# Kernel tuning notes

Measured on AMD Instinct MI355X. Metric: run time of the kernel, lower is better.

## Reference

```python
import jax, jax.numpy as jnp
import numpy as np

WINDOW = (8, 8)
NUM_HEADS = 12


def setup_inputs() -> dict:
    key = jax.random.key(0)
    k0, k1, k2 = jax.random.split(key, 3)
    B_, H, W, C = 8, 64, 64, 768
    x = jax.random.normal(k0, (B_, H * W, C), dtype=jnp.float32)
    qkv_w = jax.random.normal(k1, (3 * C, C), dtype=jnp.float32) * 0.02
    qkv_b = jnp.zeros((3 * C,), dtype=jnp.float32)
    proj_w = jax.random.normal(k2, (C, C), dtype=jnp.float32) * 0.02
    proj_b = jnp.zeros((C,), dtype=jnp.float32)
    return {"x": x, "qkv_w": qkv_w, "qkv_b": qkv_b,
            "proj_w": proj_w, "proj_b": proj_b, "H": H, "W": W}


def reference(x, qkv_w, qkv_b, proj_w, proj_b, H, W):
    ws0, ws1 = WINDOW
    nh = NUM_HEADS
    B_, N, C = x.shape
    hd = C // nh
    scale = hd ** (-0.5)

    x = x.reshape(B_, H, W, C)
    # pad bottom/right so H, W divisible by window size (static Python ints)
    pad_b = (ws0 - H % ws0) % ws0
    pad_r = (ws1 - W % ws1) % ws1
    x = jnp.pad(x, ((0, 0), (0, pad_b), (0, pad_r), (0, 0)))
    Hp, Wp = H + pad_b, W + pad_r

    # window partition: (B, Hp, Wp, C) -> (B*nW, ws0*ws1, C)
    xw = (x.reshape(B_, Hp // ws0, ws0, Wp // ws1, ws1, C)
            .transpose(0, 1, 3, 2, 4, 5)
            .reshape(-1, ws0 * ws1, C))
    Bw, Nw = xw.shape[0], xw.shape[1]

    # fused qkv projection
    qkv = xw @ qkv_w.T + qkv_b                       # (Bw, Nw, 3C)
    qkv = qkv.reshape(Bw, Nw, 3, nh, hd).transpose(2, 0, 3, 1, 4)
    q, k, v = qkv[0], qkv[1], qkv[2]                 # (Bw, nh, Nw, hd)

    attn = jax.nn.softmax((q * scale) @ jnp.swapaxes(k, -2, -1), axis=-1)
    out = (attn @ v).transpose(0, 2, 1, 3).reshape(Bw, Nw, C)
    out = out @ proj_w.T + proj_b

    # window reverse: (B*nW, ws0*ws1, C) -> (B, Hp, Wp, C)
    out = (out.reshape(B_, Hp // ws0, Wp // ws1, ws0, ws1, C)
              .transpose(0, 1, 3, 2, 4, 5)
              .reshape(B_, Hp, Wp, C))
    out = out[:, :H, :W, :]
    return out.reshape(B_, H * W, C)
```

## Files before the change

kernel.cpp:

```cpp
#include <hip/hip_runtime.h>
#include <stdint.h>

typedef __attribute__((ext_vector_type(8))) __bf16 bf16x8;
typedef __attribute__((ext_vector_type(4))) float f32x4;
typedef __attribute__((ext_vector_type(8))) unsigned short u16x8;
typedef __attribute__((ext_vector_type(2))) unsigned int u32x2;

__device__ __forceinline__ unsigned short f2bf(float f) {
  union { float f; unsigned u; } v; v.f = f;
  return (unsigned short)((v.u + 0x7FFFu + ((v.u >> 16) & 1u)) >> 16);
}

__device__ __forceinline__ void gload16(const void* g, void* l) {
  __builtin_amdgcn_global_load_lds(
      (const __attribute__((address_space(1))) void*)g,
      (__attribute__((address_space(3))) void*)l, 16, 0, 0);
}

__global__ __launch_bounds__(256) void pack_x_kernel(const float* __restrict__ x,
                                                     unsigned short* __restrict__ xw) {
  int idx = blockIdx.x * 256 + threadIdx.x;
  int m = idx / 96;
  int p = idx - m * 96;
  int win = m >> 6, tok = m & 63;
  int b = win >> 6, wh = (win >> 3) & 7, ww = win & 7;
  int r = tok >> 3, c = tok & 7;
  size_t xoff = ((size_t)b * 4096 + (wh * 8 + r) * 64 + (ww * 8 + c)) * 768 + p * 8;
  const float* src = x + xoff;
  u16x8 o;
#pragma unroll
  for (int j = 0; j < 8; ++j) o[j] = f2bf(src[j]);
  *(u16x8*)(xw + (size_t)m * 768 + p * 8) = o;
}

__global__ __launch_bounds__(256) void pack_w_kernel(const float* __restrict__ qkvw,
                                                     const float* __restrict__ projw,
                                                     unsigned short* __restrict__ wq,
                                                     unsigned short* __restrict__ wp) {
  int idx = blockIdx.x * 256 + threadIdx.x;
  const float* src;
  unsigned short* dst;
  if (idx < 221184) { src = qkvw + (size_t)idx * 8; dst = wq + (size_t)idx * 8; }
  else { int i2 = idx - 221184; src = projw + (size_t)i2 * 8; dst = wp + (size_t)i2 * 8; }
  u16x8 o;
#pragma unroll
  for (int j = 0; j < 8; ++j) o[j] = f2bf(src[j]);
  *(u16x8*)dst = o;
}

template <int N, bool PROJ>
__global__ __launch_bounds__(512, 2) void gemm256_kernel(
    const unsigned short* __restrict__ A, const unsigned short* __restrict__ Bm,
    const float* __restrict__ bias, void* __restrict__ Cout) {
  constexpr int K = 768;
  constexpr int NT = K / 32;
  constexpr int NBN = N / 256;
  extern __shared__ char smem[];

  const int tid = threadIdx.x;
  const int wave = tid >> 6;
  const int lane = tid & 63;
  const int wm = wave >> 2;
  const int wn = wave & 3;

  const int cpx = gridDim.x >> 3;
  const int bid = (blockIdx.x & 7) * cpx + (blockIdx.x >> 3);
  const int tm = (bid / NBN) * 256;
  const int tn = (bid % NBN) * 256;

  const int c0 = tid, c1 = 512 + tid;
  const int r0 = c0 >> 2, r1 = c1 >> 2;
  const int g0 = ((c0 & 3) ^ ((c0 >> 3) & 3)) * 8;
  const int g1 = ((c1 & 3) ^ ((c1 >> 3) & 3)) * 8;
  const unsigned short* gA0 = A + (size_t)(tm + r0) * K + g0;
  const unsigned short* gA1 = A + (size_t)(tm + r1) * K + g1;
  const unsigned short* gB0 = Bm + (size_t)(tn + r0) * K + g0;
  const unsigned short* gB1 = Bm + (size_t)(tn + r1) * K + g1;
  const int ldsA0 = wave * 1024;
  const int ldsA1 = 8192 + wave * 1024;
  const int ldsB0 = 16384 + wave * 1024;
  const int ldsB1 = 24576 + wave * 1024;

  const int lrow = lane & 15;
  const int lg8 = ((lane >> 4) ^ ((lane >> 1) & 3)) * 8;

  {
    char* s0 = smem;
    char* s1 = smem + 32768;
    gload16(gA0, s0 + ldsA0); gload16(gA1, s0 + ldsA1);
    gload16(gB0, s0 + ldsB0); gload16(gB1, s0 + ldsB1);
    gload16(gA0 + 32, s1 + ldsA0); gload16(gA1 + 32, s1 + ldsA1);
    gload16(gB0 + 32, s1 + ldsB0); gload16(gB1 + 32, s1 + ldsB1);
  }
  asm volatile("s_waitcnt vmcnt(4)" ::: "memory");
  asm volatile("s_barrier" ::: "memory");

  f32x4 acc[8][4] = {};

  bf16x8 a0[4], b[4];
  {
    const unsigned short* s0 = (const unsigned short*)smem;
#pragma unroll
    for (int mi = 0; mi < 4; ++mi)
      a0[mi] = *(const bf16x8*)(s0 + (wm * 128 + mi * 16 + lrow) * 32 + lg8);
#pragma unroll
    for (int ni = 0; ni < 4; ++ni)
      b[ni] = *(const bf16x8*)(s0 + 8192 + (wn * 64 + ni * 16 + lrow) * 32 + lg8);
  }

#pragma unroll
  for (int t = 0; t < NT; ++t) {
    const unsigned short* sAt = (const unsigned short*)(smem + ((t & 3) << 15));

    if (t + 2 < NT) {
      char* sb = smem + (((t + 2) & 3) << 15);
      gload16(gA0 + (t + 2) * 32, sb + ldsA0);
      gload16(gA1 + (t + 2) * 32, sb + ldsA1);
    }
    bf16x8 a1[4];
#pragma unroll
    for (int mi = 0; mi < 4; ++mi)
      a1[mi] = *(const bf16x8*)(sAt + (wm * 128 + 64 + mi * 16 + lrow) * 32 + lg8);

    __builtin_amdgcn_s_setprio(1);
#pragma unroll
    for (int mi = 0; mi < 4; ++mi)
#pragma unroll
      for (int ni = 0; ni < 4; ++ni)
        acc[mi][ni] = __builtin_amdgcn_mfma_f32_16x16x32_bf16(b[ni], a0[mi], acc[mi][ni], 0, 0, 0);
    __builtin_amdgcn_s_setprio(0);

    if (t + 2 < NT) {
      char* sb = smem + (((t + 2) & 3) << 15);
      gload16(gB0 + (t + 2) * 32, sb + ldsB0);
      gload16(gB1 + (t + 2) * 32, sb + ldsB1);
    }
    if (t < NT - 2)
      asm volatile("s_waitcnt vmcnt(4)" ::: "memory");
    else if (t == NT - 2)
      asm volatile("s_waitcnt vmcnt(0)" ::: "memory");
    if (t < NT - 1)
      asm volatile("s_barrier" ::: "memory");

    bf16x8 a0n[4], bn[4];
    if (t + 1 < NT) {
      const unsigned short* sN = (const unsigned short*)(smem + (((t + 1) & 3) << 15));
#pragma unroll
      for (int mi = 0; mi < 4; ++mi)
        a0n[mi] = *(const bf16x8*)(sN + (wm * 128 + mi * 16 + lrow) * 32 + lg8);
#pragma unroll
      for (int ni = 0; ni < 4; ++ni)
        bn[ni] = *(const bf16x8*)(sN + 8192 + (wn * 64 + ni * 16 + lrow) * 32 + lg8);
    }

    __builtin_amdgcn_s_setprio(1);
#pragma unroll
    for (int mi = 0; mi < 4; ++mi)
#pragma unroll
      for (int ni = 0; ni < 4; ++ni)
        acc[4 + mi][ni] = __builtin_amdgcn_mfma_f32_16x16x32_bf16(b[ni], a1[mi], acc[4 + mi][ni], 0, 0, 0);
    __builtin_amdgcn_s_setprio(0);

#pragma unroll
    for (int i = 0; i < 4; ++i) { a0[i] = a0n[i]; b[i] = bn[i]; }
  }

  const int erow = tm + wm * 128 + (lane & 15);
  const int ecol = tn + wn * 64 + ((lane >> 4) << 2);
  if constexpr (!PROJ) {
    unsigned short* C = (unsigned short*)Cout;
#pragma unroll
    for (int ni = 0; ni < 4; ++ni) {
      const int col0 = ecol + ni * 16;
      const f32x4 bv = *(const f32x4*)&bias[col0];
#pragma unroll
      for (int mi = 0; mi < 8; ++mi) {
        f32x4 v = acc[mi][ni];
        u32x2 pk;
        pk.x = (unsigned)f2bf(v[0] + bv[0]) | ((unsigned)f2bf(v[1] + bv[1]) << 16);
        pk.y = (unsigned)f2bf(v[2] + bv[2]) | ((unsigned)f2bf(v[3] + bv[3]) << 16);
        *(u32x2*)(C + (size_t)(erow + mi * 16) * N + col0) = pk;
      }
    }
  } else {
    float* out = (float*)Cout;
    f32x4 bv[4];
#pragma unroll
    for (int ni = 0; ni < 4; ++ni) bv[ni] = *(const f32x4*)&bias[ecol + ni * 16];
#pragma unroll
    for (int mi = 0; mi < 8; ++mi) {
      int m = erow + mi * 16;
      int win = m >> 6, tok = m & 63;
      int bb = win >> 6, wh = (win >> 3) & 7, ww = win & 7;
      int rr = tok >> 3, cc = tok & 7;
      float* op = out + ((size_t)bb * 4096 + (wh * 8 + rr) * 64 + (ww * 8 + cc)) * 768;
#pragma unroll
      for (int ni = 0; ni < 4; ++ni) {
        f32x4 o = acc[mi][ni] + bv[ni];
        *(f32x4*)(op + ecol + ni * 16) = o;
      }
    }
  }
}

__global__ __launch_bounds__(64) void attn_kernel(const unsigned short* __restrict__ qkv,
                                                  unsigned short* __restrict__ attnout) {
  __shared__ unsigned short sQ[64 * 64];
  __shared__ unsigned short sK[64 * 64];
  __shared__ unsigned short sVT[64 * 64];
  const int lane = threadIdx.x;
  const int win = blockIdx.x / 12;
  const int head = blockIdx.x - win * 12;
  const size_t row0 = (size_t)win * 64;
  const int qoff = head * 64, koff = 768 + head * 64, voff = 1536 + head * 64;

#pragma unroll
  for (int i = 0; i < 8; ++i) {
    int e = lane + i * 64;
    int row = e >> 3, cb = (e & 7) * 8;
    gload16(qkv + (row0 + row) * 2304 + qoff + cb, (char*)sQ + i * 1024);
    gload16(qkv + (row0 + row) * 2304 + koff + cb, (char*)sK + i * 1024);
  }
  {
    const unsigned short* gv = qkv + (row0 + lane) * 2304 + voff;
#pragma unroll
    for (int j = 0; j < 8; ++j) {
      u16x8 v = *(const u16x8*)(gv + j * 8);
#pragma unroll
      for (int d = 0; d < 8; ++d) sVT[(j * 8 + d) * 64 + lane] = v[d];
    }
  }
  __syncthreads();

  const int lrow = lane & 15;
  const int lkb = (lane >> 4) * 8;

  f32x4 s[4][4] = {};
#pragma unroll
  for (int ks = 0; ks < 2; ++ks) {
    bf16x8 qf[4], kf[4];
#pragma unroll
    for (int mi = 0; mi < 4; ++mi) qf[mi] = *(const bf16x8*)&sQ[(mi * 16 + lrow) * 64 + ks * 32 + lkb];
#pragma unroll
    for (int ni = 0; ni < 4; ++ni) kf[ni] = *(const bf16x8*)&sK[(ni * 16 + lrow) * 64 + ks * 32 + lkb];
#pragma unroll
    for (int mi = 0; mi < 4; ++mi)
#pragma unroll
      for (int ni = 0; ni < 4; ++ni)
        s[mi][ni] = __builtin_amdgcn_mfma_f32_16x16x32_bf16(qf[mi], kf[ni], s[mi][ni], 0, 0, 0);
  }

  float p[4][4][4];
#pragma unroll
  for (int mi = 0; mi < 4; ++mi) {
#pragma unroll
    for (int r = 0; r < 4; ++r) {
      float v0 = s[mi][0][r] * 0.125f, v1 = s[mi][1][r] * 0.125f;
      float v2 = s[mi][2][r] * 0.125f, v3 = s[mi][3][r] * 0.125f;
      float mx = fmaxf(fmaxf(v0, v1), fmaxf(v2, v3));
      mx = fmaxf(mx, __shfl_xor(mx, 1));
      mx = fmaxf(mx, __shfl_xor(mx, 2));
      mx = fmaxf(mx, __shfl_xor(mx, 4));
      mx = fmaxf(mx, __shfl_xor(mx, 8));
      float e0 = __expf(v0 - mx), e1 = __expf(v1 - mx);
      float e2 = __expf(v2 - mx), e3 = __expf(v3 - mx);
      float sm = e0 + e1 + e2 + e3;
      sm += __shfl_xor(sm, 1);
      sm += __shfl_xor(sm, 2);
      sm += __shfl_xor(sm, 4);
      sm += __shfl_xor(sm, 8);
      float inv = 1.0f / sm;
      p[mi][0][r] = e0 * inv; p[mi][1][r] = e1 * inv;
      p[mi][2][r] = e2 * inv; p[mi][3][r] = e3 * inv;
    }
  }

  __syncthreads();
#pragma unroll
  for (int mi = 0; mi < 4; ++mi)
#pragma unroll
    for (int ni = 0; ni < 4; ++ni)
#pragma unroll
      for (int r = 0; r < 4; ++r)
        sK[(mi * 16 + (lane >> 4) * 4 + r) * 64 + ni * 16 + lrow] = f2bf(p[mi][ni][r]);
  __syncthreads();

  f32x4 o[4][4] = {};
#pragma unroll
  for (int ks = 0; ks < 2; ++ks) {
    bf16x8 pf[4], vf[4];
#pragma unroll
    for (int mi = 0; mi < 4; ++mi) pf[mi] = *(const bf16x8*)&sK[(mi * 16 + lrow) * 64 + ks * 32 + lkb];
#pragma unroll
    for (int ni = 0; ni < 4; ++ni) vf[ni] = *(const bf16x8*)&sVT[(ni * 16 + lrow) * 64 + ks * 32 + lkb];
#pragma unroll
    for (int mi = 0; mi < 4; ++mi)
#pragma unroll
      for (int ni = 0; ni < 4; ++ni)
        o[mi][ni] = __builtin_amdgcn_mfma_f32_16x16x32_bf16(pf[mi], vf[ni], o[mi][ni], 0, 0, 0);
  }

#pragma unroll
  for (int mi = 0; mi < 4; ++mi)
#pragma unroll
    for (int ni = 0; ni < 4; ++ni) {
      int col = head * 64 + ni * 16 + lrow;
#pragma unroll
      for (int r = 0; r < 4; ++r) {
        int trow = mi * 16 + (lane >> 4) * 4 + r;
        attnout[(row0 + trow) * 768 + col] = f2bf(o[mi][ni][r]);
      }
    }
}

extern "C" void kernel_launch(void* const* d_in, const int* in_sizes, int n_in,
                              void* d_out, int out_size, void* d_ws, size_t ws_size,
                              hipStream_t stream) {
  (void)in_sizes; (void)n_in; (void)out_size; (void)ws_size;
  const float* x = (const float*)d_in[0];
  const float* qkv_w = (const float*)d_in[1];
  const float* qkv_b = (const float*)d_in[2];
  const float* proj_w = (const float*)d_in[3];
  const float* proj_b = (const float*)d_in[4];
  float* out = (float*)d_out;

  char* ws = (char*)d_ws;
  unsigned short* xw   = (unsigned short*)(ws);
  unsigned short* qkvB = (unsigned short*)(ws + 50331648);
  unsigned short* wq   = (unsigned short*)(ws + 50331648 + 150994944);
  unsigned short* wp   = (unsigned short*)(ws + 50331648 + 150994944 + 3538944);

  (void)hipFuncSetAttribute((const void*)(gemm256_kernel<2304, false>),
                            hipFuncAttributeMaxDynamicSharedMemorySize, 131072);
  (void)hipFuncSetAttribute((const void*)(gemm256_kernel<768, true>),
                            hipFuncAttributeMaxDynamicSharedMemorySize, 131072);

  pack_x_kernel<<<12288, 256, 0, stream>>>(x, xw);
  pack_w_kernel<<<1152, 256, 0, stream>>>(qkv_w, proj_w, wq, wp);
  gemm256_kernel<2304, false><<<1152, 512, 131072, stream>>>(xw, wq, qkv_b, qkvB);
  attn_kernel<<<6144, 64, 0, stream>>>(qkvB, xw);
  gemm256_kernel<768, true><<<384, 512, 131072, stream>>>(xw, wp, proj_b, out);
}
```

Before: 282.7 us.

## Restructure GEMM main loop to 64-wide K steps with barrier-phased MFMA quadrants

The GEMM's K-step doubles from 32 to 64, and the four-slot, two-ahead prefetch ring becomes a two-slot, one-ahead double buffer of 64KB stages loaded with a new XOR-swizzled global-to-LDS pattern. Each step is split into four MFMA quadrants separated by workgroup barriers, with LDS fragment loads interleaved between them, in a ping-pong style schedule. The aim is to halve the number of outer iterations and waits and to overlap LDS reads with matrix work across waves. The cost is many more s_barrier instructions per step and a shallower prefetch distance, which can expose global load latency.

```diff
diff --git a/kernel.cpp b/kernel.cpp
--- a/kernel.cpp
+++ b/kernel.cpp
@@ -53,7 +53,7 @@
     const unsigned short* __restrict__ A, const unsigned short* __restrict__ Bm,
     const float* __restrict__ bias, void* __restrict__ Cout) {
   constexpr int K = 768;
-  constexpr int NT = K / 32;
+  constexpr int NSTEP = K / 64;
   constexpr int NBN = N / 256;
   extern __shared__ char smem[];
 
@@ -68,102 +68,121 @@
   const int tm = (bid / NBN) * 256;
   const int tn = (bid % NBN) * 256;
 
-  const int c0 = tid, c1 = 512 + tid;
-  const int r0 = c0 >> 2, r1 = c1 >> 2;
-  const int g0 = ((c0 & 3) ^ ((c0 >> 3) & 3)) * 8;
-  const int g1 = ((c1 & 3) ^ ((c1 >> 3) & 3)) * 8;
-  const unsigned short* gA0 = A + (size_t)(tm + r0) * K + g0;
-  const unsigned short* gA1 = A + (size_t)(tm + r1) * K + g1;
-  const unsigned short* gB0 = Bm + (size_t)(tn + r0) * K + g0;
-  const unsigned short* gB1 = Bm + (size_t)(tn + r1) * K + g1;
-  const int ldsA0 = wave * 1024;
-  const int ldsA1 = 8192 + wave * 1024;
-  const int ldsB0 = 16384 + wave * 1024;
-  const int ldsB1 = 24576 + wave * 1024;
+  const int rb = (wave << 3) + (lane >> 3);
+  const int sg = ((lane & 7) ^ (lane >> 3)) * 8;
+  const unsigned short* gA = A + (size_t)(tm + rb) * K + sg;
+  const unsigned short* gB = Bm + (size_t)(tn + rb) * K + sg;
+  const int ldsW = wave * 1024;
+
+#define STAGE(s, bsel) do {                                              \
+    char* d_ = smem + ((bsel) << 16);                                    \
+    const unsigned short* a_ = gA + (s) * 64;                            \
+    const unsigned short* b_ = gB + (s) * 64;                            \
+    gload16(a_,                d_ + ldsW);                               \
+    gload16(a_ + (size_t)64*K, d_ + 8192 + ldsW);                        \
+    gload16(a_ + (size_t)128*K, d_ + 16384 + ldsW);                      \
+    gload16(a_ + (size_t)192*K, d_ + 24576 + ldsW);                      \
+    gload16(b_,                d_ + 32768 + ldsW);                       \
+    gload16(b_ + (size_t)64*K, d_ + 40960 + ldsW);                       \
+    gload16(b_ + (size_t)128*K, d_ + 49152 + ldsW);                      \
+    gload16(b_ + (size_t)192*K, d_ + 57344 + ldsW);                      \
+  } while (0)
 
   const int lrow = lane & 15;
-  const int lg8 = ((lane >> 4) ^ ((lane >> 1) & 3)) * 8;
-
-  {
-    char* s0 = smem;
-    char* s1 = smem + 32768;
-    gload16(gA0, s0 + ldsA0); gload16(gA1, s0 + ldsA1);
-    gload16(gB0, s0 + ldsB0); gload16(gB1, s0 + ldsB1);
-    gload16(gA0 + 32, s1 + ldsA0); gload16(gA1 + 32, s1 + ldsA1);
-    gload16(gB0 + 32, s1 + ldsB0); gload16(gB1 + 32, s1 + ldsB1);
-  }
-  asm volatile("s_waitcnt vmcnt(4)" ::: "memory");
-  asm volatile("s_barrier" ::: "memory");
+  const int pg0b = (((lane >> 4) ^ (lane & 7)) << 4);
+
+  STAGE(0, 0);
 
   f32x4 acc[8][4] = {};
 
-  bf16x8 a0[4], b[4];
-  {
-    const unsigned short* s0 = (const unsigned short*)smem;
-#pragma unroll
-    for (int mi = 0; mi < 4; ++mi)
-      a0[mi] = *(const bf16x8*)(s0 + (wm * 128 + mi * 16 + lrow) * 32 + lg8);
-#pragma unroll
-    for (int ni = 0; ni < 4; ++ni)
-      b[ni] = *(const bf16x8*)(s0 + 8192 + (wn * 64 + ni * 16 + lrow) * 32 + lg8);
-  }
-
-#pragma unroll
-  for (int t = 0; t < NT; ++t) {
-    const unsigned short* sAt = (const unsigned short*)(smem + ((t & 3) << 15));
-
-    if (t + 2 < NT) {
-      char* sb = smem + (((t + 2) & 3) << 15);
-      gload16(gA0 + (t + 2) * 32, sb + ldsA0);
-      gload16(gA1 + (t + 2) * 32, sb + ldsA1);
-    }
-    bf16x8 a1[4];
-#pragma unroll
-    for (int mi = 0; mi < 4; ++mi)
-      a1[mi] = *(const bf16x8*)(sAt + (wm * 128 + 64 + mi * 16 + lrow) * 32 + lg8);
-
+  for (int t = 0; t < NSTEP; ++t) {
+    if (t + 1 < NSTEP) {
+      STAGE(t + 1, (t + 1) & 1);
+      asm volatile("s_waitcnt vmcnt(8)" ::: "memory");
+    } else {
+      asm volatile("s_waitcnt vmcnt(0)" ::: "memory");
+    }
+    asm volatile("s_barrier" ::: "memory");
+
+    const char* cb = smem + ((t & 1) << 16);
+    const char* aB = cb + wm * 16384 + lrow * 128;
+    const char* bB = cb + 32768 + (wn >> 1) * 16384 + ((wn & 1) * 64 + lrow) * 128;
+
+    bf16x8 a0[8], a1[8], be[4], bo[4];
+
+#pragma unroll
+    for (int mi = 0; mi < 4; ++mi)
+#pragma unroll
+      for (int kh = 0; kh < 2; ++kh)
+        a0[mi * 2 + kh] = *(const bf16x8*)(aB + (mi * 16) * 128 + (pg0b ^ (kh << 6)));
+#pragma unroll
+    for (int ni = 0; ni < 2; ++ni)
+#pragma unroll
+      for (int kh = 0; kh < 2; ++kh)
+        be[ni * 2 + kh] = *(const bf16x8*)(bB + (ni * 16) * 128 + (pg0b ^ (kh << 6)));
+    asm volatile("s_barrier" ::: "memory");
     __builtin_amdgcn_s_setprio(1);
 #pragma unroll
     for (int mi = 0; mi < 4; ++mi)
 #pragma unroll
-      for (int ni = 0; ni < 4; ++ni)
-        acc[mi][ni] = __builtin_amdgcn_mfma_f32_16x16x32_bf16(b[ni], a0[mi], acc[mi][ni], 0, 0, 0);
+      for (int ni = 0; ni < 2; ++ni)
+#pragma unroll
+        for (int kh = 0; kh < 2; ++kh)
+          acc[mi][ni] = __builtin_amdgcn_mfma_f32_16x16x32_bf16(
+              be[ni * 2 + kh], a0[mi * 2 + kh], acc[mi][ni], 0, 0, 0);
     __builtin_amdgcn_s_setprio(0);
-
-    if (t + 2 < NT) {
-      char* sb = smem + (((t + 2) & 3) << 15);
-      gload16(gB0 + (t + 2) * 32, sb + ldsB0);
-      gload16(gB1 + (t + 2) * 32, sb + ldsB1);
-    }
-    if (t < NT - 2)
-      asm volatile("s_waitcnt vmcnt(4)" ::: "memory");
-    else if (t == NT - 2)
-      asm volatile("s_waitcnt vmcnt(0)" ::: "memory");
-    if (t < NT - 1)
-      asm volatile("s_barrier" ::: "memory");
-
-    bf16x8 a0n[4], bn[4];
-    if (t + 1 < NT) {
-      const unsigned short* sN = (const unsigned short*)(smem + (((t + 1) & 3) << 15));
-#pragma unroll
-      for (int mi = 0; mi < 4; ++mi)
-        a0n[mi] = *(const bf16x8*)(sN + (wm * 128 + mi * 16 + lrow) * 32 + lg8);
-#pragma unroll
-      for (int ni = 0; ni < 4; ++ni)
-        bn[ni] = *(const bf16x8*)(sN + 8192 + (wn * 64 + ni * 16 + lrow) * 32 + lg8);
-    }
-
+    asm volatile("s_barrier" ::: "memory");
+
+#pragma unroll
+    for (int ni = 0; ni < 2; ++ni)
+#pragma unroll
+      for (int kh = 0; kh < 2; ++kh)
+        bo[ni * 2 + kh] = *(const bf16x8*)(bB + ((ni + 2) * 16) * 128 + (pg0b ^ (kh << 6)));
+    asm volatile("s_barrier" ::: "memory");
     __builtin_amdgcn_s_setprio(1);
 #pragma unroll
     for (int mi = 0; mi < 4; ++mi)
 #pragma unroll
-      for (int ni = 0; ni < 4; ++ni)
-        acc[4 + mi][ni] = __builtin_amdgcn_mfma_f32_16x16x32_bf16(b[ni], a1[mi], acc[4 + mi][ni], 0, 0, 0);
+      for (int ni = 0; ni < 2; ++ni)
+#pragma unroll
+        for (int kh = 0; kh < 2; ++kh)
+          acc[mi][ni + 2] = __builtin_amdgcn_mfma_f32_16x16x32_bf16(
+              bo[ni * 2 + kh], a0[mi * 2 + kh], acc[mi][ni + 2], 0, 0, 0);
     __builtin_amdgcn_s_setprio(0);
-
-#pragma unroll
-    for (int i = 0; i < 4; ++i) { a0[i] = a0n[i]; b[i] = bn[i]; }
-  }
+    asm volatile("s_barrier" ::: "memory");
+
+#pragma unroll
+    for (int mi = 0; mi < 4; ++mi)
+#pragma unroll
+      for (int kh = 0; kh < 2; ++kh)
+        a1[mi * 2 + kh] = *(const bf16x8*)(aB + ((64 + mi * 16)) * 128 + (pg0b ^ (kh << 6)));
+    asm volatile("s_barrier" ::: "memory");
+    __builtin_amdgcn_s_setprio(1);
+#pragma unroll
+    for (int mi = 0; mi < 4; ++mi)
+#pragma unroll
+      for (int ni = 0; ni < 2; ++ni)
+#pragma unroll
+        for (int kh = 0; kh < 2; ++kh)
+          acc[4 + mi][ni + 2] = __builtin_amdgcn_mfma_f32_16x16x32_bf16(
+              bo[ni * 2 + kh], a1[mi * 2 + kh], acc[4 + mi][ni + 2], 0, 0, 0);
+    __builtin_amdgcn_s_setprio(0);
+    asm volatile("s_barrier" ::: "memory");
+
+    asm volatile("s_barrier" ::: "memory");
+    __builtin_amdgcn_s_setprio(1);
+#pragma unroll
+    for (int mi = 0; mi < 4; ++mi)
+#pragma unroll
+      for (int ni = 0; ni < 2; ++ni)
+#pragma unroll
+        for (int kh = 0; kh < 2; ++kh)
+          acc[4 + mi][ni] = __builtin_amdgcn_mfma_f32_16x16x32_bf16(
+              be[ni * 2 + kh], a1[mi * 2 + kh], acc[4 + mi][ni], 0, 0, 0);
+    __builtin_amdgcn_s_setprio(0);
+    asm volatile("s_barrier" ::: "memory");
+  }
+#undef STAGE
 
   const int erow = tm + wm * 128 + (lane & 15);
   const int ecol = tn + wn * 64 + ((lane >> 4) << 2);
```

Result: slower. 300.3 us (+6.2%).

## Shrink GEMM tiles to 128x128 with 4 waves and triple-buffered LDS

Applied to the files above, without the earlier changes.

Replaces the 256x256-tile, 512-thread GEMM with a 128x128-tile, 256-thread variant that uses 48KB of static LDS split into three 16KB stages, instead of four 32KB stages of dynamic LDS. Each wave now computes a 64x64 sub-tile, and the grids grow to 4608 and 1536 blocks. The aim is higher occupancy (launch bounds of 3 blocks per CU) and better load balance and wave-tail behaviour across CUs. The cost is less operand reuse per tile, which means more global and LDS traffic per FLOP.

```diff
diff --git a/kernel.cpp b/kernel.cpp
--- a/kernel.cpp
+++ b/kernel.cpp
@@ -49,124 +49,115 @@
 }
 
 template <int N, bool PROJ>
-__global__ __launch_bounds__(512, 2) void gemm256_kernel(
+__global__ __launch_bounds__(256, 3) void gemm128_kernel(
     const unsigned short* __restrict__ A, const unsigned short* __restrict__ Bm,
     const float* __restrict__ bias, void* __restrict__ Cout) {
   constexpr int K = 768;
   constexpr int NT = K / 32;
-  constexpr int NBN = N / 256;
-  extern __shared__ char smem[];
+  constexpr int NBN = N / 128;
+  __shared__ char smem[49152];
 
   const int tid = threadIdx.x;
   const int wave = tid >> 6;
   const int lane = tid & 63;
-  const int wm = wave >> 2;
-  const int wn = wave & 3;
+  const int wmr = wave >> 1;
+  const int wnc = wave & 1;
 
   const int cpx = gridDim.x >> 3;
   const int bid = (blockIdx.x & 7) * cpx + (blockIdx.x >> 3);
-  const int tm = (bid / NBN) * 256;
-  const int tn = (bid % NBN) * 256;
-
-  const int c0 = tid, c1 = 512 + tid;
-  const int r0 = c0 >> 2, r1 = c1 >> 2;
-  const int g0 = ((c0 & 3) ^ ((c0 >> 3) & 3)) * 8;
-  const int g1 = ((c1 & 3) ^ ((c1 >> 3) & 3)) * 8;
-  const unsigned short* gA0 = A + (size_t)(tm + r0) * K + g0;
-  const unsigned short* gA1 = A + (size_t)(tm + r1) * K + g1;
-  const unsigned short* gB0 = Bm + (size_t)(tn + r0) * K + g0;
-  const unsigned short* gB1 = Bm + (size_t)(tn + r1) * K + g1;
-  const int ldsA0 = wave * 1024;
-  const int ldsA1 = 8192 + wave * 1024;
-  const int ldsB0 = 16384 + wave * 1024;
-  const int ldsB1 = 24576 + wave * 1024;
+  const int tm = (bid / NBN) * 128;
+  const int tn = (bid % NBN) * 128;
+
+  const int srow0 = wave * 16 + (lane >> 2);
+  const int sgl = ((lane & 3) ^ ((lane >> 3) & 3)) * 8;
+  const unsigned short* gA0 = A + (size_t)(tm + srow0) * K + sgl;
+  const unsigned short* gA1 = A + (size_t)(tm + 64 + srow0) * K + sgl;
+  const unsigned short* gB0 = Bm + (size_t)(tn + srow0) * K + sgl;
+  const unsigned short* gB1 = Bm + (size_t)(tn + 64 + srow0) * K + sgl;
+  const int ldsW = wave * 1024;
+
+#define STAGE(s, slot) do {                                        \
+    char* d_ = smem + (slot) * 16384;                              \
+    gload16(gA0 + (s) * 32, d_ + ldsW);                            \
+    gload16(gA1 + (s) * 32, d_ + 4096 + ldsW);                     \
+    gload16(gB0 + (s) * 32, d_ + 8192 + ldsW);                     \
+    gload16(gB1 + (s) * 32, d_ + 12288 + ldsW);                    \
+  } while (0)
 
   const int lrow = lane & 15;
-  const int lg8 = ((lane >> 4) ^ ((lane >> 1) & 3)) * 8;
-
-  {
-    char* s0 = smem;
-    char* s1 = smem + 32768;
-    gload16(gA0, s0 + ldsA0); gload16(gA1, s0 + ldsA1);
-    gload16(gB0, s0 + ldsB0); gload16(gB1, s0 + ldsB1);
-    gload16(gA0 + 32, s1 + ldsA0); gload16(gA1 + 32, s1 + ldsA1);
-    gload16(gB0 + 32, s1 + ldsB0); gload16(gB1 + 32, s1 + ldsB1);
-  }
+  const int pgb = (((lane >> 4) ^ ((lane >> 1) & 3)) << 4);
+
+  STAGE(0, 0);
+  STAGE(1, 1);
   asm volatile("s_waitcnt vmcnt(4)" ::: "memory");
   asm volatile("s_barrier" ::: "memory");
 
-  f32x4 acc[8][4] = {};
-
-  bf16x8 a0[4], b[4];
+  f32x4 acc[4][4] = {};
+
+  bf16x8 a0[2], b[4];
   {
-    const unsigned short* s0 = (const unsigned short*)smem;
-#pragma unroll
-    for (int mi = 0; mi < 4; ++mi)
-      a0[mi] = *(const bf16x8*)(s0 + (wm * 128 + mi * 16 + lrow) * 32 + lg8);
-#pragma unroll
-    for (int ni = 0; ni < 4; ++ni)
-      b[ni] = *(const bf16x8*)(s0 + 8192 + (wn * 64 + ni * 16 + lrow) * 32 + lg8);
+    const char* aB = smem + (wmr * 64 + lrow) * 64 + pgb;
+    const char* bB = smem + 8192 + (wnc * 64 + lrow) * 64 + pgb;
+#pragma unroll
+    for (int mi = 0; mi < 2; ++mi) a0[mi] = *(const bf16x8*)(aB + mi * 1024);
+#pragma unroll
+    for (int ni = 0; ni < 4; ++ni) b[ni] = *(const bf16x8*)(bB + ni * 1024);
   }
 
 #pragma unroll
   for (int t = 0; t < NT; ++t) {
-    const unsigned short* sAt = (const unsigned short*)(smem + ((t & 3) << 15));
-
-    if (t + 2 < NT) {
-      char* sb = smem + (((t + 2) & 3) << 15);
-      gload16(gA0 + (t + 2) * 32, sb + ldsA0);
-      gload16(gA1 + (t + 2) * 32, sb + ldsA1);
-    }
-    bf16x8 a1[4];
-#pragma unroll
-    for (int mi = 0; mi < 4; ++mi)
-      a1[mi] = *(const bf16x8*)(sAt + (wm * 128 + 64 + mi * 16 + lrow) * 32 + lg8);
+    const char* cb = smem + (t % 3) * 16384;
+    const char* aB = cb + (wmr * 64 + lrow) * 64 + pgb;
+
+    if (t + 2 < NT) STAGE(t + 2, (t + 2) % 3);
+    bf16x8 a1[2];
+#pragma unroll
+    for (int mi = 0; mi < 2; ++mi)
+      a1[mi] = *(const bf16x8*)(aB + (2 + mi) * 1024);
 
     __builtin_amdgcn_s_setprio(1);
 #pragma unroll
-    for (int mi = 0; mi < 4; ++mi)
+    for (int mi = 0; mi < 2; ++mi)
 #pragma unroll
       for (int ni = 0; ni < 4; ++ni)
         acc[mi][ni] = __builtin_amdgcn_mfma_f32_16x16x32_bf16(b[ni], a0[mi], acc[mi][ni], 0, 0, 0);
     __builtin_amdgcn_s_setprio(0);
 
-    if (t + 2 < NT) {
-      char* sb = smem + (((t + 2) & 3) << 15);
-      gload16(gB0 + (t + 2) * 32, sb + ldsB0);
-      gload16(gB1 + (t + 2) * 32, sb + ldsB1);
-    }
-    if (t < NT - 2)
+    if (t + 2 < NT)
       asm volatile("s_waitcnt vmcnt(4)" ::: "memory");
     else if (t == NT - 2)
       asm volatile("s_waitcnt vmcnt(0)" ::: "memory");
-    if (t < NT - 1)
+    if (t + 1 < NT)
       asm volatile("s_barrier" ::: "memory");
 
-    bf16x8 a0n[4], bn[4];
+    bf16x8 a0n[2], bn[4];
     if (t + 1 < NT) {
-      const unsigned short* sN = (const unsigned short*)(smem + (((t + 1) & 3) << 15));
-#pragma unroll
-      for (int mi = 0; mi < 4; ++mi)
-        a0n[mi] = *(const bf16x8*)(sN + (wm * 128 + mi * 16 + lrow) * 32 + lg8);
+      const char* nb = smem + ((t + 1) % 3) * 16384;
+      const char* aN = nb + (wmr * 64 + lrow) * 64 + pgb;
+      const char* bN = nb + 8192 + (wnc * 64 + lrow) * 64 + pgb;
+#pragma unroll
+      for (int mi = 0; mi < 2; ++mi) a0n[mi] = *(const bf16x8*)(aN + mi * 1024);
+#pragma unroll
+      for (int ni = 0; ni < 4; ++ni) bn[ni] = *(const bf16x8*)(bN + ni * 1024);
+    }
+
+    __builtin_amdgcn_s_setprio(1);
+#pragma unroll
+    for (int mi = 0; mi < 2; ++mi)
 #pragma unroll
       for (int ni = 0; ni < 4; ++ni)
-        bn[ni] = *(const bf16x8*)(sN + 8192 + (wn * 64 + ni * 16 + lrow) * 32 + lg8);
-    }
-
-    __builtin_amdgcn_s_setprio(1);
-#pragma unroll
-    for (int mi = 0; mi < 4; ++mi)
-#pragma unroll
-      for (int ni = 0; ni < 4; ++ni)
-        acc[4 + mi][ni] = __builtin_amdgcn_mfma_f32_16x16x32_bf16(b[ni], a1[mi], acc[4 + mi][ni], 0, 0, 0);
+        acc[2 + mi][ni] = __builtin_amdgcn_mfma_f32_16x16x32_bf16(b[ni], a1[mi], acc[2 + mi][ni], 0, 0, 0);
     __builtin_amdgcn_s_setprio(0);
 
 #pragma unroll
-    for (int i = 0; i < 4; ++i) { a0[i] = a0n[i]; b[i] = bn[i]; }
-  }
-
-  const int erow = tm + wm * 128 + (lane & 15);
-  const int ecol = tn + wn * 64 + ((lane >> 4) << 2);
+    for (int i = 0; i < 2; ++i) a0[i] = a0n[i];
+#pragma unroll
+    for (int i = 0; i < 4; ++i) b[i] = bn[i];
+  }
+#undef STAGE
+
+  const int erow = tm + wmr * 64 + (lane & 15);
+  const int ecol = tn + wnc * 64 + ((lane >> 4) << 2);
   if constexpr (!PROJ) {
     unsigned short* C = (unsigned short*)Cout;
 #pragma unroll
@@ -174,7 +165,7 @@
       const int col0 = ecol + ni * 16;
       const f32x4 bv = *(const f32x4*)&bias[col0];
 #pragma unroll
-      for (int mi = 0; mi < 8; ++mi) {
+      for (int mi = 0; mi < 4; ++mi) {
         f32x4 v = acc[mi][ni];
         u32x2 pk;
         pk.x = (unsigned)f2bf(v[0] + bv[0]) | ((unsigned)f2bf(v[1] + bv[1]) << 16);
@@ -188,7 +179,7 @@
 #pragma unroll
     for (int ni = 0; ni < 4; ++ni) bv[ni] = *(const f32x4*)&bias[ecol + ni * 16];
 #pragma unroll
-    for (int mi = 0; mi < 8; ++mi) {
+    for (int mi = 0; mi < 4; ++mi) {
       int m = erow + mi * 16;
       int win = m >> 6, tok = m & 63;
       int bb = win >> 6, wh = (win >> 3) & 7, ww = win & 7;
@@ -330,14 +321,9 @@
   unsigned short* wq   = (unsigned short*)(ws + 50331648 + 150994944);
   unsigned short* wp   = (unsigned short*)(ws + 50331648 + 150994944 + 3538944);
 
-  (void)hipFuncSetAttribute((const void*)(gemm256_kernel<2304, false>),
-                            hipFuncAttributeMaxDynamicSharedMemorySize, 131072);
-  (void)hipFuncSetAttribute((const void*)(gemm256_kernel<768, true>),
-                            hipFuncAttributeMaxDynamicSharedMemorySize, 131072);
-
   pack_x_kernel<<<12288, 256, 0, stream>>>(x, xw);
   pack_w_kernel<<<1152, 256, 0, stream>>>(qkv_w, proj_w, wq, wp);
-  gemm256_kernel<2304, false><<<1152, 512, 131072, stream>>>(xw, wq, qkv_b, qkvB);
+  gemm128_kernel<2304, false><<<4608, 256, 0, stream>>>(xw, wq, qkv_b, qkvB);
   attn_kernel<<<6144, 64, 0, stream>>>(qkvB, xw);
-  gemm256_kernel<768, true><<<384, 512, 131072, stream>>>(xw, wp, proj_b, out);
-}
+  gemm128_kernel<768, true><<<1536, 256, 0, stream>>>(xw, wp, proj_b, out);
+}
```

Measured after the change: 296.5 us. 1.05x slower.

## Use 128x128 tiled kernel with 3-stage pipeline for output projection GEMM

Applied to the files above, without the earlier changes.

The output projection GEMM now runs in a dedicated 128x128-tile kernel with 256 threads and a triple-buffered LDS pipeline, launched on 1536 blocks instead of 384 blocks of 256x256 tiles. The goal is to fill the GPU with more workgroups: 384 large tiles leave many CUs idle or underused. The QKV GEMM epilogue is also simplified by hoisting bias loads and reordering loops. In exchange, each smaller tile re-reads more A and B data from global memory.

```diff
diff --git a/kernel.cpp b/kernel.cpp
--- a/kernel.cpp
+++ b/kernel.cpp
@@ -6,9 +6,9 @@
 typedef __attribute__((ext_vector_type(8))) unsigned short u16x8;
 typedef __attribute__((ext_vector_type(2))) unsigned int u32x2;
 
-__device__ __forceinline__ unsigned short f2bf(float f) {
+__device__ __forceinline__ unsigned f2bf(float f) {
   union { float f; unsigned u; } v; v.f = f;
-  return (unsigned short)((v.u + 0x7FFFu + ((v.u >> 16) & 1u)) >> 16);
+  return (v.u + 0x7FFFu + ((v.u >> 16) & 1u)) >> 16;
 }
 
 __device__ __forceinline__ void gload16(const void* g, void* l) {
@@ -29,7 +29,7 @@
   const float* src = x + xoff;
   u16x8 o;
 #pragma unroll
-  for (int j = 0; j < 8; ++j) o[j] = f2bf(src[j]);
+  for (int j = 0; j < 8; ++j) o[j] = (unsigned short)f2bf(src[j]);
   *(u16x8*)(xw + (size_t)m * 768 + p * 8) = o;
 }
 
@@ -44,14 +44,14 @@
   else { int i2 = idx - 221184; src = projw + (size_t)i2 * 8; dst = wp + (size_t)i2 * 8; }
   u16x8 o;
 #pragma unroll
-  for (int j = 0; j < 8; ++j) o[j] = f2bf(src[j]);
+  for (int j = 0; j < 8; ++j) o[j] = (unsigned short)f2bf(src[j]);
   *(u16x8*)dst = o;
 }
 
-template <int N, bool PROJ>
+template <int N>
 __global__ __launch_bounds__(512, 2) void gemm256_kernel(
     const unsigned short* __restrict__ A, const unsigned short* __restrict__ Bm,
-    const float* __restrict__ bias, void* __restrict__ Cout) {
+    const float* __restrict__ bias, unsigned short* __restrict__ C) {
   constexpr int K = 768;
   constexpr int NT = K / 32;
   constexpr int NBN = N / 256;
@@ -167,38 +167,147 @@
 
   const int erow = tm + wm * 128 + (lane & 15);
   const int ecol = tn + wn * 64 + ((lane >> 4) << 2);
-  if constexpr (!PROJ) {
-    unsigned short* C = (unsigned short*)Cout;
+  f32x4 bv[4];
+#pragma unroll
+  for (int ni = 0; ni < 4; ++ni) bv[ni] = *(const f32x4*)&bias[ecol + ni * 16];
+#pragma unroll
+  for (int mi = 0; mi < 8; ++mi) {
+    unsigned short* rowp = C + (size_t)(erow + mi * 16) * N;
 #pragma unroll
     for (int ni = 0; ni < 4; ++ni) {
-      const int col0 = ecol + ni * 16;
-      const f32x4 bv = *(const f32x4*)&bias[col0];
-#pragma unroll
-      for (int mi = 0; mi < 8; ++mi) {
-        f32x4 v = acc[mi][ni];
-        u32x2 pk;
-        pk.x = (unsigned)f2bf(v[0] + bv[0]) | ((unsigned)f2bf(v[1] + bv[1]) << 16);
-        pk.y = (unsigned)f2bf(v[2] + bv[2]) | ((unsigned)f2bf(v[3] + bv[3]) << 16);
-        *(u32x2*)(C + (size_t)(erow + mi * 16) * N + col0) = pk;
-      }
-    }
-  } else {
-    float* out = (float*)Cout;
-    f32x4 bv[4];
-#pragma unroll
-    for (int ni = 0; ni < 4; ++ni) bv[ni] = *(const f32x4*)&bias[ecol + ni * 16];
-#pragma unroll
-    for (int mi = 0; mi < 8; ++mi) {
-      int m = erow + mi * 16;
-      int win = m >> 6, tok = m & 63;
-      int bb = win >> 6, wh = (win >> 3) & 7, ww = win & 7;
-      int rr = tok >> 3, cc = tok & 7;
-      float* op = out + ((size_t)bb * 4096 + (wh * 8 + rr) * 64 + (ww * 8 + cc)) * 768;
-#pragma unroll
-      for (int ni = 0; ni < 4; ++ni) {
-        f32x4 o = acc[mi][ni] + bv[ni];
-        *(f32x4*)(op + ecol + ni * 16) = o;
-      }
+      f32x4 v = acc[mi][ni];
+      u32x2 pk;
+      pk.x = f2bf(v[0] + bv[ni][0]) | (f2bf(v[1] + bv[ni][1]) << 16);
+      pk.y = f2bf(v[2] + bv[ni][2]) | (f2bf(v[3] + bv[ni][3]) << 16);
+      *(u32x2*)(rowp + ecol + ni * 16) = pk;
+    }
+  }
+}
+
+__global__ __launch_bounds__(256, 3) void gemm128_proj_kernel(
+    const unsigned short* __restrict__ A, const unsigned short* __restrict__ Bm,
+    const float* __restrict__ bias, float* __restrict__ out) {
+  constexpr int K = 768;
+  constexpr int NT = K / 32;
+  constexpr int N = 768;
+  constexpr int NBN = N / 128;
+  __shared__ char smem[49152];
+
+  const int tid = threadIdx.x;
+  const int wave = tid >> 6;
+  const int lane = tid & 63;
+  const int wmr = wave >> 1;
+  const int wnc = wave & 1;
+
+  const int cpx = gridDim.x >> 3;
+  const int bid = (blockIdx.x & 7) * cpx + (blockIdx.x >> 3);
+  const int tm = (bid / NBN) * 128;
+  const int tn = (bid % NBN) * 128;
+
+  const int srow0 = wave * 16 + (lane >> 2);
+  const int sgl = ((lane & 3) ^ ((lane >> 3) & 3)) * 8;
+  const unsigned short* gA0 = A + (size_t)(tm + srow0) * K + sgl;
+  const unsigned short* gA1 = A + (size_t)(tm + 64 + srow0) * K + sgl;
+  const unsigned short* gB0 = Bm + (size_t)(tn + srow0) * K + sgl;
+  const unsigned short* gB1 = Bm + (size_t)(tn + 64 + srow0) * K + sgl;
+  const int ldsW = wave * 1024;
+
+#define STAGE(s, slot) do {                                        \
+    char* d_ = smem + (slot) * 16384;                              \
+    gload16(gA0 + (s) * 32, d_ + ldsW);                            \
+    gload16(gA1 + (s) * 32, d_ + 4096 + ldsW);                     \
+    gload16(gB0 + (s) * 32, d_ + 8192 + ldsW);                     \
+    gload16(gB1 + (s) * 32, d_ + 12288 + ldsW);                    \
+  } while (0)
+
+  const int lrow = lane & 15;
+  const int pgb = (((lane >> 4) ^ ((lane >> 1) & 3)) << 4);
+
+  STAGE(0, 0);
+  STAGE(1, 1);
+  asm volatile("s_waitcnt vmcnt(4)" ::: "memory");
+  asm volatile("s_barrier" ::: "memory");
+
+  f32x4 acc[4][4] = {};
+
+  bf16x8 a0[2], b[4];
+  {
+    const char* aB = smem + (wmr * 64 + lrow) * 64 + pgb;
+    const char* bB = smem + 8192 + (wnc * 64 + lrow) * 64 + pgb;
+#pragma unroll
+    for (int mi = 0; mi < 2; ++mi) a0[mi] = *(const bf16x8*)(aB + mi * 1024);
+#pragma unroll
+    for (int ni = 0; ni < 4; ++ni) b[ni] = *(const bf16x8*)(bB + ni * 1024);
+  }
+
+#pragma unroll
+  for (int t = 0; t < NT; ++t) {
+    const char* cb = smem + (t % 3) * 16384;
+    const char* aB = cb + (wmr * 64 + lrow) * 64 + pgb;
+
+    if (t + 2 < NT) STAGE(t + 2, (t + 2) % 3);
+    bf16x8 a1[2];
+#pragma unroll
+    for (int mi = 0; mi < 2; ++mi)
+      a1[mi] = *(const bf16x8*)(aB + (2 + mi) * 1024);
+
+    __builtin_amdgcn_s_setprio(1);
+#pragma unroll
+    for (int mi = 0; mi < 2; ++mi)
+#pragma unroll
+      for (int ni = 0; ni < 4; ++ni)
+        acc[mi][ni] = __builtin_amdgcn_mfma_f32_16x16x32_bf16(b[ni], a0[mi], acc[mi][ni], 0, 0, 0);
+    __builtin_amdgcn_s_setprio(0);
+
+    if (t + 2 < NT)
+      asm volatile("s_waitcnt vmcnt(4)" ::: "memory");
+    else if (t == NT - 2)
+      asm volatile("s_waitcnt vmcnt(0)" ::: "memory");
+    if (t + 1 < NT)
+      asm volatile("s_barrier" ::: "memory");
+
+    bf16x8 a0n[2], bn[4];
+    if (t + 1 < NT) {
+      const char* nb = smem + ((t + 1) % 3) * 16384;
+      const char* aN = nb + (wmr * 64 + lrow) * 64 + pgb;
+      const char* bN = nb + 8192 + (wnc * 64 + lrow) * 64 + pgb;
+#pragma unroll
+      for (int mi = 0; mi < 2; ++mi) a0n[mi] = *(const bf16x8*)(aN + mi * 1024);
+#pragma unroll
+      for (int ni = 0; ni < 4; ++ni) bn[ni] = *(const bf16x8*)(bN + ni * 1024);
+    }
+
+    __builtin_amdgcn_s_setprio(1);
+#pragma unroll
+    for (int mi = 0; mi < 2; ++mi)
+#pragma unroll
+      for (int ni = 0; ni < 4; ++ni)
+        acc[2 + mi][ni] = __builtin_amdgcn_mfma_f32_16x16x32_bf16(b[ni], a1[mi], acc[2 + mi][ni], 0, 0, 0);
+    __builtin_amdgcn_s_setprio(0);
+
+#pragma unroll
+    for (int i = 0; i < 2; ++i) a0[i] = a0n[i];
+#pragma unroll
+    for (int i = 0; i < 4; ++i) b[i] = bn[i];
+  }
+#undef STAGE
+
+  const int erow = tm + wmr * 64 + (lane & 15);
+  const int ecol = tn + wnc * 64 + ((lane >> 4) << 2);
+  f32x4 bv[4];
+#pragma unroll
+  for (int ni = 0; ni < 4; ++ni) bv[ni] = *(const f32x4*)&bias[ecol + ni * 16];
+#pragma unroll
+  for (int mi = 0; mi < 4; ++mi) {
+    int m = erow + mi * 16;
+    int win = m >> 6, tok = m & 63;
+    int bb = win >> 6, wh = (win >> 3) & 7, ww = win & 7;
+    int rr = tok >> 3, cc = tok & 7;
+    float* op = out + ((size_t)bb * 4096 + (wh * 8 + rr) * 64 + (ww * 8 + cc)) * 768;
+#pragma unroll
+    for (int ni = 0; ni < 4; ++ni) {
+      f32x4 o = acc[mi][ni] + bv[ni];
+      *(f32x4*)(op + ecol + ni * 16) = o;
     }
   }
 }
@@ -282,7 +391,7 @@
     for (int ni = 0; ni < 4; ++ni)
 #pragma unroll
       for (int r = 0; r < 4; ++r)
-        sK[(mi * 16 + (lane >> 4) * 4 + r) * 64 + ni * 16 + lrow] = f2bf(p[mi][ni][r]);
+        sK[(mi * 16 + (lane >> 4) * 4 + r) * 64 + ni * 16 + lrow] = (unsigned short)f2bf(p[mi][ni][r]);
   __syncthreads();
 
   f32x4 o[4][4] = {};
@@ -308,7 +417,7 @@
 #pragma unroll
       for (int r = 0; r < 4; ++r) {
         int trow = mi * 16 + (lane >> 4) * 4 + r;
-        attnout[(row0 + trow) * 768 + col] = f2bf(o[mi][ni][r]);
+        attnout[(row0 + trow) * 768 + col] = (unsigned short)f2bf(o[mi][ni][r]);
       }
     }
 }
@@ -330,14 +439,12 @@
   unsigned short* wq   = (unsigned short*)(ws + 50331648 + 150994944);
   unsigned short* wp   = (unsigned short*)(ws + 50331648 + 150994944 + 3538944);
 
-  (void)hipFuncSetAttribute((const void*)(gemm256_kernel<2304, false>),
-                            hipFuncAttributeMaxDynamicSharedMemorySize, 131072);
-  (void)hipFuncSetAttribute((const void*)(gemm256_kernel<768, true>),
+  (void)hipFuncSetAttribute((const void*)(gemm256_kernel<2304>),
                             hipFuncAttributeMaxDynamicSharedMemorySize, 131072);
 
   pack_x_kernel<<<12288, 256, 0, stream>>>(x, xw);
   pack_w_kernel<<<1152, 256, 0, stream>>>(qkv_w, proj_w, wq, wp);
-  gemm256_kernel<2304, false><<<1152, 512, 131072, stream>>>(xw, wq, qkv_b, qkvB);
+  gemm256_kernel<2304><<<1152, 512, 131072, stream>>>(xw, wq, qkv_b, qkvB);
   attn_kernel<<<6144, 64, 0, stream>>>(qkvB, xw);
-  gemm256_kernel<768, true><<<384, 512, 131072, stream>>>(xw, wp, proj_b, out);
-}
+  gemm128_proj_kernel<<<1536, 256, 0, stream>>>(xw, wp, proj_b, out);
+}
```

Result: no change. 285.2 us (+0.9%).
